# Performance work log

Measured on AMD Instinct MI355X. Metric: run time of the kernel, lower is better.

The kernel has to match this reference:

```python
import jax, jax.numpy as jnp
import numpy as np

DIM = 1024
HEADS = 16

def setup_inputs() -> dict:
    key = jax.random.key(0)
    k1, k2, k3, k4 = jax.random.split(key, 4)
    x = jax.random.normal(k1, (2, 2048, DIM), dtype=jnp.float32)
    ln_gamma = jnp.ones((DIM,), dtype=jnp.float32)
    ln_beta = jnp.zeros((DIM,), dtype=jnp.float32)
    # torch Linear weight is [out, in]; store transposed [in, out] for x @ W
    W_qkv = jax.random.normal(k2, (DIM, 3 * DIM), dtype=jnp.float32) * (DIM ** -0.5)
    W_out = jax.random.normal(k3, (DIM, DIM), dtype=jnp.float32) * (DIM ** -0.5)
    b_out = jax.random.normal(k4, (DIM,), dtype=jnp.float32) * 0.02
    return {"x": x, "ln_gamma": ln_gamma, "ln_beta": ln_beta,
            "W_qkv": W_qkv, "W_out": W_out, "b_out": b_out}

def reference(x, ln_gamma, ln_beta, W_qkv, W_out, b_out):
    B, N, C = x.shape
    H = HEADS
    Dh = C // H
    scale = Dh ** -0.5
    # LayerNorm (eps=1e-5, torch default)
    mu = jnp.mean(x, axis=-1, keepdims=True)
    var = jnp.var(x, axis=-1, keepdims=True)
    xn = (x - mu) / jnp.sqrt(var + 1e-5) * ln_gamma + ln_beta
    # QKV projection: [B,N,3C] -> [3,B,H,N,Dh]
    qkv = (xn @ W_qkv).reshape(B, N, 3, H, Dh).transpose(2, 0, 3, 1, 4)
    q, k, v = qkv[0], qkv[1], qkv[2]
    attn = jnp.einsum('bhnd,bhmd->bhnm', q, k) * scale  # [B,H,N,N]
    attn = jax.nn.softmax(attn, axis=-1)
    out = jnp.einsum('bhnm,bhmd->bhnd', attn, v)  # [B,H,N,Dh]
    out = out.transpose(0, 2, 1, 3).reshape(B, N, C)
    return out @ W_out + b_out
```

## Files before the change

kernel.cpp:

```cpp
#include <hip/hip_runtime.h>
#include <hip/hip_bf16.h>

#define DIM 1024
#define HEADS 16
#define DH 64
#define SEQ 2048
#define BATCH 2
#define ROWS (BATCH*SEQ)
#define C3 (3*DIM)
#define NT (SEQ/64)

typedef __attribute__((ext_vector_type(8))) short s16x8;
typedef __attribute__((ext_vector_type(4))) short s16x4;
typedef __attribute__((ext_vector_type(4))) float f32x4;
typedef __attribute__((ext_vector_type(16))) float f32x16;
typedef __attribute__((ext_vector_type(4))) unsigned int u32x4;
typedef __attribute__((ext_vector_type(2))) unsigned int u32x2;

__device__ __forceinline__ void gll16(const void* g, void* l) {
  __builtin_amdgcn_global_load_lds((const __attribute__((address_space(1))) void*)g,
                                   (__attribute__((address_space(3))) void*)l, 16, 0, 0);
}
__device__ __forceinline__ float bf2f(short s) {
  return __builtin_bit_cast(float, ((unsigned)(unsigned short)s) << 16);
}
__device__ __forceinline__ short f2bf(float f) {
  return (short)__bfloat16_as_ushort(__float2bfloat16(f));
}
__device__ __forceinline__ unsigned pk2(float a, float b) {
  unsigned lo = (unsigned)__bfloat16_as_ushort(__float2bfloat16(a));
  unsigned hh = (unsigned)__bfloat16_as_ushort(__float2bfloat16(b));
  return lo | (hh << 16);
}
__device__ __forceinline__ float fexp2(float x) {
#if __has_builtin(__builtin_amdgcn_exp2f)
  return __builtin_amdgcn_exp2f(x);
#else
  float r; asm("v_exp_f32 %0, %1" : "=v"(r) : "v"(x)); return r;
#endif
}

__global__ __launch_bounds__(256) void ln_kernel(const float* __restrict__ x,
    const float* __restrict__ gamma, const float* __restrict__ beta,
    __hip_bfloat16* __restrict__ xn) {
  int row = blockIdx.x;
  int t = threadIdx.x;
  const float4* xp = (const float4*)(x + (size_t)row * DIM);
  float4 v = xp[t];
  float s = v.x + v.y + v.z + v.w;
  float q = v.x*v.x + v.y*v.y + v.z*v.z + v.w*v.w;
  for (int off = 32; off >= 1; off >>= 1) {
    s += __shfl_xor(s, off, 64);
    q += __shfl_xor(q, off, 64);
  }
  __shared__ float red[8];
  int w = t >> 6;
  if ((t & 63) == 0) { red[w] = s; red[4 + w] = q; }
  __syncthreads();
  s = red[0] + red[1] + red[2] + red[3];
  q = red[4] + red[5] + red[6] + red[7];
  float mu = s * (1.0f / DIM);
  float var = q * (1.0f / DIM) - mu * mu;
  float rstd = rsqrtf(var + 1e-5f);
  int c = t * 4;
  float4 g4 = ((const float4*)gamma)[t];
  float4 b4 = ((const float4*)beta)[t];
  __hip_bfloat16* op = xn + (size_t)row * DIM + c;
  op[0] = __float2bfloat16((v.x - mu) * rstd * g4.x + b4.x);
  op[1] = __float2bfloat16((v.y - mu) * rstd * g4.y + b4.y);
  op[2] = __float2bfloat16((v.z - mu) * rstd * g4.z + b4.z);
  op[3] = __float2bfloat16((v.w - mu) * rstd * g4.w + b4.w);
}

__global__ __launch_bounds__(256) void transpose_cvt(const float* __restrict__ in,
    __hip_bfloat16* __restrict__ out, int R, int Cn) {
  __shared__ float tile[32][33];
  int c0 = blockIdx.x * 32, r0 = blockIdx.y * 32;
  int tx = threadIdx.x & 31, ty = threadIdx.x >> 5;
#pragma unroll
  for (int i = 0; i < 4; i++)
    tile[ty + i * 8][tx] = in[(size_t)(r0 + ty + i * 8) * Cn + c0 + tx];
  __syncthreads();
#pragma unroll
  for (int i = 0; i < 4; i++)
    out[(size_t)(c0 + ty + i * 8) * R + r0 + tx] = __float2bfloat16(tile[tx][ty + i * 8]);
}

__global__ __launch_bounds__(512) void gemm192(const __hip_bfloat16* __restrict__ A,
    const __hip_bfloat16* __restrict__ Bt, __hip_bfloat16* __restrict__ C,
    int M, int Nc, int K) {
  __shared__ short lds_a[2][256 * 64];
  __shared__ short lds_b[2][192 * 64];
  const int t = threadIdx.x, l = t & 63;
  const int w = t >> 6, wr = w >> 2, wc = w & 3;
  const int m0 = blockIdx.y * 256, n0 = blockIdx.x * 192;
  const short* Ab = (const short*)A;
  const short* Bb = (const short*)Bt;
  f32x4 acc[8][3] = {};
  const int srow = t >> 3;
  const int schk = (t & 7) ^ (srow & 7);
  const int NIT = K / 64;

  {
    char* la = (char*)&lds_a[0][0];
    char* lb = (char*)&lds_b[0][0];
#pragma unroll
    for (int p = 0; p < 4; p++)
      gll16(Ab + (size_t)(m0 + p * 64 + srow) * K + schk * 8, la + p * 8192 + t * 16);
#pragma unroll
    for (int p = 0; p < 3; p++)
      gll16(Bb + (size_t)(n0 + p * 64 + srow) * K + schk * 8, lb + p * 8192 + t * 16);
  }
  for (int it = 0; it < NIT; ++it) {
    const int cur = it & 1;
    __syncthreads();
    if (it + 1 < NIT) {
      const int kk = (it + 1) * 64;
      char* la = (char*)&lds_a[cur ^ 1][0];
      char* lb = (char*)&lds_b[cur ^ 1][0];
#pragma unroll
      for (int p = 0; p < 4; p++)
        gll16(Ab + (size_t)(m0 + p * 64 + srow) * K + kk + schk * 8, la + p * 8192 + t * 16);
#pragma unroll
      for (int p = 0; p < 3; p++)
        gll16(Bb + (size_t)(n0 + p * 64 + srow) * K + kk + schk * 8, lb + p * 8192 + t * 16);
      asm volatile("s_waitcnt vmcnt(7)" ::: "memory");
    } else {
      asm volatile("s_waitcnt vmcnt(0)" ::: "memory");
    }
    __syncthreads();
    const char* la = (const char*)&lds_a[cur][0];
    const char* lb = (const char*)&lds_b[cur][0];
#pragma unroll
    for (int s = 0; s < 2; s++) {
      s16x8 af[8], bf[3];
#pragma unroll
      for (int f = 0; f < 8; f++) {
        int row = wr * 128 + f * 16 + (l & 15);
        int chk = ((s * 4 + (l >> 4)) ^ (l & 7)) * 16;
        af[f] = *(const s16x8*)(la + row * 128 + chk);
      }
#pragma unroll
      for (int n = 0; n < 3; n++) {
        int row = wc * 48 + n * 16 + (l & 15);
        int chk = ((s * 4 + (l >> 4)) ^ (l & 7)) * 16;
        bf[n] = *(const s16x8*)(lb + row * 128 + chk);
      }
#pragma unroll
      for (int f = 0; f < 8; f++)
#pragma unroll
        for (int n = 0; n < 3; n++)
          acc[f][n] = __builtin_amdgcn_mfma_f32_16x16x32_bf16(af[f], bf[n], acc[f][n], 0, 0, 0);
    }
  }
#pragma unroll
  for (int f = 0; f < 8; f++)
#pragma unroll
    for (int n = 0; n < 3; n++) {
      int col = n0 + wc * 48 + n * 16 + (l & 15);
#pragma unroll
      for (int r = 0; r < 4; r++) {
        int row = m0 + wr * 128 + f * 16 + (l >> 4) * 4 + r;
        C[(size_t)row * Nc + col] = __float2bfloat16(acc[f][n][r]);
      }
    }
}

__global__ __launch_bounds__(256) void gemm_out(const __hip_bfloat16* __restrict__ A,
    const __hip_bfloat16* __restrict__ Bt, float* __restrict__ C,
    const float* __restrict__ bias) {
  __shared__ short lds_a[2][128 * 32];
  __shared__ short lds_b[2][64 * 32];
  const int t = threadIdx.x, l = t & 63, w = t >> 6;
  const int wr = w >> 1, wc = w & 1;
  const int m0 = blockIdx.y * 128, n0 = blockIdx.x * 64;
  const short* Ab = (const short*)A;
  const short* Bb = (const short*)Bt;
  const int K = DIM;
  f32x4 acc[4][2] = {};
  const int srow = t >> 2, scol = (t & 3) * 8;
  {
    char* la = (char*)&lds_a[0][0];
    char* lb = (char*)&lds_b[0][0];
    gll16(Ab + (size_t)(m0 + srow) * K + scol,      la + t * 16);
    gll16(Ab + (size_t)(m0 + 64 + srow) * K + scol, la + 4096 + t * 16);
    gll16(Bb + (size_t)(n0 + srow) * K + scol,      lb + t * 16);
  }
  for (int it = 0; it < K / 32; ++it) {
    const int cur = it & 1;
    __syncthreads();
    if (it + 1 < K / 32) {
      const int kk = (it + 1) * 32;
      char* la = (char*)&lds_a[cur ^ 1][0];
      char* lb = (char*)&lds_b[cur ^ 1][0];
      gll16(Ab + (size_t)(m0 + srow) * K + kk + scol,      la + t * 16);
      gll16(Ab + (size_t)(m0 + 64 + srow) * K + kk + scol, la + 4096 + t * 16);
      gll16(Bb + (size_t)(n0 + srow) * K + kk + scol,      lb + t * 16);
      asm volatile("s_waitcnt vmcnt(3)" ::: "memory");
    } else {
      asm volatile("s_waitcnt vmcnt(0)" ::: "memory");
    }
    __syncthreads();
    s16x8 af[4], bf[2];
#pragma unroll
    for (int m = 0; m < 4; m++)
      af[m] = *(const s16x8*)&lds_a[cur][(wr * 64 + m * 16 + (l & 15)) * 32 + (l >> 4) * 8];
#pragma unroll
    for (int n = 0; n < 2; n++)
      bf[n] = *(const s16x8*)&lds_b[cur][(wc * 32 + n * 16 + (l & 15)) * 32 + (l >> 4) * 8];
#pragma unroll
    for (int m = 0; m < 4; m++)
#pragma unroll
      for (int n = 0; n < 2; n++)
        acc[m][n] = __builtin_amdgcn_mfma_f32_16x16x32_bf16(af[m], bf[n], acc[m][n], 0, 0, 0);
  }
#pragma unroll
  for (int m = 0; m < 4; m++)
#pragma unroll
    for (int n = 0; n < 2; n++) {
      int col = n0 + wc * 32 + n * 16 + (l & 15);
      float bb = bias[col];
#pragma unroll
      for (int r = 0; r < 4; r++) {
        int row = m0 + wr * 64 + m * 16 + (l >> 4) * 4 + r;
        C[(size_t)row * DIM + col] = acc[m][n][r] + bb;
      }
    }
}

__global__ __launch_bounds__(512) void attn_kernel(const __hip_bfloat16* __restrict__ qkv,
    __hip_bfloat16* __restrict__ attno) {
  const int t = threadIdx.x, l = t & 63, w = t >> 6;
  const int hi = l >> 5, lq = l & 31;
  const int qb = blockIdx.x, bh = blockIdx.y;
  const int b = bh >> 4, h = bh & 15;
  const short* base  = (const short*)qkv + (size_t)b * SEQ * C3 + h * DH;
  const short* kbase = base + DIM;
  const short* vbase = base + 2 * DIM;
  const int qr0 = qb * 256 + w * 32;

  __shared__ short kbuf[2][64 * 64];
  __shared__ short vbuf[2][64 * 64];

  const float SCL = 0.125f * 1.44269504089f;
  s16x8 qf[4];
#pragma unroll
  for (int dk = 0; dk < 4; dk++) {
    s16x8 raw = *(const s16x8*)(base + (size_t)(qr0 + lq) * C3 + dk * 16 + hi * 8);
#pragma unroll
    for (int j = 0; j < 8; j++) qf[dk][j] = f2bf(bf2f(raw[j]) * SCL);
  }

  s16x8 ones;
#pragma unroll
  for (int j = 0; j < 8; j++) ones[j] = (short)0x3F80;

  f32x16 o0, o1, osum;
#pragma unroll
  for (int r = 0; r < 16; r++) { o0[r] = 0.f; o1[r] = 0.f; osum[r] = 0.f; }

  const int krow = t >> 3;
  const int ksrc = (t & 7) ^ (krow & 7);
  const int vr = t & 31, vcg = t >> 5;

  {
    gll16(kbase + (size_t)krow * C3 + ksrc * 8, (char*)&kbuf[0][0] + t * 16);
    u32x2 vau = __builtin_bit_cast(u32x2, *(const s16x4*)(vbase + (size_t)(2 * vr) * C3 + vcg * 4));
    u32x2 vbu = __builtin_bit_cast(u32x2, *(const s16x4*)(vbase + (size_t)(2 * vr + 1) * C3 + vcg * 4));
    char* vd = (char*)&vbuf[0][0];
#pragma unroll
    for (int i = 0; i < 4; i++) {
      int d = vcg * 4 + i;
      unsigned dw = __builtin_amdgcn_perm(vbu[i >> 1], vau[i >> 1],
                                          (i & 1) ? 0x07060302u : 0x05040100u);
      *(unsigned*)(vd + d * 128 + (((vr >> 2) ^ (d & 7)) * 16) + (vr & 3) * 4) = dw;
    }
  }
  __syncthreads();

  for (int tile = 0; tile < NT; ++tile) {
    const int cur = tile & 1;
    const bool pf = (tile + 1 < NT);
    u32x2 vau, vbu;
    if (pf) {
      const int kv1 = (tile + 1) * 64;
      gll16(kbase + (size_t)(kv1 + krow) * C3 + ksrc * 8, (char*)&kbuf[cur ^ 1][0] + t * 16);
      vau = __builtin_bit_cast(u32x2, *(const s16x4*)(vbase + (size_t)(kv1 + 2 * vr) * C3 + vcg * 4));
      vbu = __builtin_bit_cast(u32x2, *(const s16x4*)(vbase + (size_t)(kv1 + 2 * vr + 1) * C3 + vcg * 4));
    }
    const char* kb = (const char*)&kbuf[cur][0];
    f32x16 st0, st1;
#pragma unroll
    for (int r = 0; r < 16; r++) { st0[r] = 0.f; st1[r] = 0.f; }
#pragma unroll
    for (int dk = 0; dk < 4; dk++) {
      int chk = ((2 * dk + hi) ^ (l & 7)) * 16;
      s16x8 kf0 = *(const s16x8*)(kb + (size_t)lq * 128 + chk);
      s16x8 kf1 = *(const s16x8*)(kb + (size_t)(32 + lq) * 128 + chk);
      st0 = __builtin_amdgcn_mfma_f32_32x32x16_bf16(kf0, qf[dk], st0, 0, 0, 0);
      st1 = __builtin_amdgcn_mfma_f32_32x32x16_bf16(kf1, qf[dk], st1, 0, 0, 0);
    }
#pragma unroll
    for (int r = 0; r < 16; r++) {
      st0[r] = fexp2(st0[r]);
      st1[r] = fexp2(st1[r]);
    }
    const char* vbp = (const char*)&vbuf[cur][0];
#pragma unroll
    for (int n = 0; n < 2; n++) {
      const f32x16& stn = n ? st1 : st0;
#pragma unroll
      for (int ksl = 0; ksl < 2; ksl++) {
        int rb = ksl * 8;
        int a  = (int)pk2(stn[rb + 0], stn[rb + 1]);
        int bq = (int)pk2(stn[rb + 2], stn[rb + 3]);
        int c  = (int)pk2(stn[rb + 4], stn[rb + 5]);
        int d  = (int)pk2(stn[rb + 6], stn[rb + 7]);
        asm volatile("v_permlane32_swap_b32 %0, %1" : "+v"(a), "+v"(c));
        asm volatile("v_permlane32_swap_b32 %0, %1" : "+v"(bq), "+v"(d));
        u32x4 fr;
        fr.x = (unsigned)a;  fr.y = (unsigned)bq;
        fr.z = (unsigned)c;  fr.w = (unsigned)d;
        s16x8 pa = __builtin_bit_cast(s16x8, fr);
        int ks = n * 2 + ksl;
        int chk = ((2 * ks + hi) ^ (l & 7)) * 16;
        s16x8 vf0 = *(const s16x8*)(vbp + (size_t)lq * 128 + chk);
        s16x8 vf1 = *(const s16x8*)(vbp + (size_t)(32 + lq) * 128 + chk);
        o0   = __builtin_amdgcn_mfma_f32_32x32x16_bf16(pa, vf0, o0, 0, 0, 0);
        o1   = __builtin_amdgcn_mfma_f32_32x32x16_bf16(pa, vf1, o1, 0, 0, 0);
        osum = __builtin_amdgcn_mfma_f32_32x32x16_bf16(pa, ones, osum, 0, 0, 0);
      }
    }
    if (pf) {
      char* vd = (char*)&vbuf[cur ^ 1][0];
#pragma unroll
      for (int i = 0; i < 4; i++) {
        int d = vcg * 4 + i;
        unsigned dw = __builtin_amdgcn_perm(vbu[i >> 1], vau[i >> 1],
                                            (i & 1) ? 0x07060302u : 0x05040100u);
        *(unsigned*)(vd + d * 128 + (((vr >> 2) ^ (d & 7)) * 16) + (vr & 3) * 4) = dw;
      }
    }
    __syncthreads();
  }
#pragma unroll
  for (int r = 0; r < 16; r++) {
    int qr = (r & 3) + 8 * (r >> 2) + 4 * hi;
    float ir = 1.0f / osum[r];
    size_t rowoff = (size_t)(b * SEQ + qr0 + qr) * DIM + h * DH;
    attno[rowoff + lq]      = __float2bfloat16(o0[r] * ir);
    attno[rowoff + 32 + lq] = __float2bfloat16(o1[r] * ir);
  }
}

extern "C" void kernel_launch(void* const* d_in, const int* in_sizes, int n_in,
                              void* d_out, int out_size, void* d_ws, size_t ws_size,
                              hipStream_t stream) {
  const float* x     = (const float*)d_in[0];
  const float* gamma = (const float*)d_in[1];
  const float* beta  = (const float*)d_in[2];
  const float* Wqkv  = (const float*)d_in[3];
  const float* Wout  = (const float*)d_in[4];
  const float* bout  = (const float*)d_in[5];

  __hip_bfloat16* xn     = (__hip_bfloat16*)d_ws;
  __hip_bfloat16* wqkv_t = xn + (size_t)ROWS * DIM;
  __hip_bfloat16* wout_t = wqkv_t + (size_t)C3 * DIM;
  __hip_bfloat16* qkv    = wout_t + (size_t)DIM * DIM;
  __hip_bfloat16* attno  = qkv + (size_t)ROWS * C3;

  ln_kernel<<<ROWS, 256, 0, stream>>>(x, gamma, beta, xn);
  transpose_cvt<<<dim3(C3 / 32, DIM / 32), 256, 0, stream>>>(Wqkv, wqkv_t, DIM, C3);
  transpose_cvt<<<dim3(DIM / 32, DIM / 32), 256, 0, stream>>>(Wout, wout_t, DIM, DIM);
  gemm192<<<dim3(C3 / 192, ROWS / 256), 512, 0, stream>>>(xn, wqkv_t, qkv, ROWS, C3, DIM);
  attn_kernel<<<dim3(SEQ / 256, BATCH * HEADS), 512, 0, stream>>>(qkv, attno);
  gemm_out<<<dim3(DIM / 64, ROWS / 128), 256, 0, stream>>>(attno, wout_t, (float*)d_out, bout);
}
```

Measured before the change: 126.0 us.

## Merge prep kernels into one launch and split QKV GEMM inner loop into phased halves

Combines the LayerNorm and both weight transpose-convert kernels into a single prep launch, dispatching on block index, to remove two kernel launches and their gaps. Separately restructures the QKV GEMM's per-tile compute into four phases, each reading half the A fragments and then issuing MFMAs under barriers with raised wave priority. This lowers live fragment registers and interleaves LDS reads with MFMA across waves, at the cost of extra barriers per K-step.

```diff
diff --git a/kernel.cpp b/kernel.cpp
--- a/kernel.cpp
+++ b/kernel.cpp
@@ -40,50 +40,59 @@
 #endif
 }
 
-__global__ __launch_bounds__(256) void ln_kernel(const float* __restrict__ x,
+__global__ __launch_bounds__(256) void prep_kernel(const float* __restrict__ x,
     const float* __restrict__ gamma, const float* __restrict__ beta,
-    __hip_bfloat16* __restrict__ xn) {
-  int row = blockIdx.x;
-  int t = threadIdx.x;
-  const float4* xp = (const float4*)(x + (size_t)row * DIM);
-  float4 v = xp[t];
-  float s = v.x + v.y + v.z + v.w;
-  float q = v.x*v.x + v.y*v.y + v.z*v.z + v.w*v.w;
-  for (int off = 32; off >= 1; off >>= 1) {
-    s += __shfl_xor(s, off, 64);
-    q += __shfl_xor(q, off, 64);
-  }
-  __shared__ float red[8];
-  int w = t >> 6;
-  if ((t & 63) == 0) { red[w] = s; red[4 + w] = q; }
-  __syncthreads();
-  s = red[0] + red[1] + red[2] + red[3];
-  q = red[4] + red[5] + red[6] + red[7];
-  float mu = s * (1.0f / DIM);
-  float var = q * (1.0f / DIM) - mu * mu;
-  float rstd = rsqrtf(var + 1e-5f);
-  int c = t * 4;
-  float4 g4 = ((const float4*)gamma)[t];
-  float4 b4 = ((const float4*)beta)[t];
-  __hip_bfloat16* op = xn + (size_t)row * DIM + c;
-  op[0] = __float2bfloat16((v.x - mu) * rstd * g4.x + b4.x);
-  op[1] = __float2bfloat16((v.y - mu) * rstd * g4.y + b4.y);
-  op[2] = __float2bfloat16((v.z - mu) * rstd * g4.z + b4.z);
-  op[3] = __float2bfloat16((v.w - mu) * rstd * g4.w + b4.w);
-}
-
-__global__ __launch_bounds__(256) void transpose_cvt(const float* __restrict__ in,
-    __hip_bfloat16* __restrict__ out, int R, int Cn) {
-  __shared__ float tile[32][33];
-  int c0 = blockIdx.x * 32, r0 = blockIdx.y * 32;
-  int tx = threadIdx.x & 31, ty = threadIdx.x >> 5;
-#pragma unroll
-  for (int i = 0; i < 4; i++)
-    tile[ty + i * 8][tx] = in[(size_t)(r0 + ty + i * 8) * Cn + c0 + tx];
-  __syncthreads();
-#pragma unroll
-  for (int i = 0; i < 4; i++)
-    out[(size_t)(c0 + ty + i * 8) * R + r0 + tx] = __float2bfloat16(tile[tx][ty + i * 8]);
+    __hip_bfloat16* __restrict__ xn,
+    const float* __restrict__ Wqkv, __hip_bfloat16* __restrict__ wqkv_t,
+    const float* __restrict__ Wout, __hip_bfloat16* __restrict__ wout_t) {
+  const int bid = blockIdx.x;
+  const int t = threadIdx.x;
+  if (bid < ROWS) {
+    __shared__ float red[8];
+    const float4* xp = (const float4*)(x + (size_t)bid * DIM);
+    float4 v = xp[t];
+    float s = v.x + v.y + v.z + v.w;
+    float q = v.x*v.x + v.y*v.y + v.z*v.z + v.w*v.w;
+    for (int off = 32; off >= 1; off >>= 1) {
+      s += __shfl_xor(s, off, 64);
+      q += __shfl_xor(q, off, 64);
+    }
+    int w = t >> 6;
+    if ((t & 63) == 0) { red[w] = s; red[4 + w] = q; }
+    __syncthreads();
+    s = red[0] + red[1] + red[2] + red[3];
+    q = red[4] + red[5] + red[6] + red[7];
+    float mu = s * (1.0f / DIM);
+    float var = q * (1.0f / DIM) - mu * mu;
+    float rstd = rsqrtf(var + 1e-5f);
+    float4 g4 = ((const float4*)gamma)[t];
+    float4 b4 = ((const float4*)beta)[t];
+    __hip_bfloat16* op = xn + (size_t)bid * DIM + t * 4;
+    op[0] = __float2bfloat16((v.x - mu) * rstd * g4.x + b4.x);
+    op[1] = __float2bfloat16((v.y - mu) * rstd * g4.y + b4.y);
+    op[2] = __float2bfloat16((v.z - mu) * rstd * g4.z + b4.z);
+    op[3] = __float2bfloat16((v.w - mu) * rstd * g4.w + b4.w);
+  } else {
+    __shared__ float tile[32][33];
+    const float* in; __hip_bfloat16* out; int R, Cn, c0, r0;
+    if (bid < ROWS + 3072) {
+      int id = bid - ROWS;
+      in = Wqkv; out = wqkv_t; R = DIM; Cn = C3;
+      c0 = (id % 96) * 32; r0 = (id / 96) * 32;
+    } else {
+      int id = bid - ROWS - 3072;
+      in = Wout; out = wout_t; R = DIM; Cn = DIM;
+      c0 = (id % 32) * 32; r0 = (id / 32) * 32;
+    }
+    int tx = t & 31, ty = t >> 5;
+#pragma unroll
+    for (int i = 0; i < 4; i++)
+      tile[ty + i * 8][tx] = in[(size_t)(r0 + ty + i * 8) * Cn + c0 + tx];
+    __syncthreads();
+#pragma unroll
+    for (int i = 0; i < 4; i++)
+      out[(size_t)(c0 + ty + i * 8) * R + r0 + tx] = __float2bfloat16(tile[tx][ty + i * 8]);
+  }
 }
 
 __global__ __launch_bounds__(512) void gemm192(const __hip_bfloat16* __restrict__ A,
@@ -131,27 +140,43 @@
     __syncthreads();
     const char* la = (const char*)&lds_a[cur][0];
     const char* lb = (const char*)&lds_b[cur][0];
-#pragma unroll
-    for (int s = 0; s < 2; s++) {
-      s16x8 af[8], bf[3];
-#pragma unroll
-      for (int f = 0; f < 8; f++) {
-        int row = wr * 128 + f * 16 + (l & 15);
-        int chk = ((s * 4 + (l >> 4)) ^ (l & 7)) * 16;
-        af[f] = *(const s16x8*)(la + row * 128 + chk);
-      }
-#pragma unroll
-      for (int n = 0; n < 3; n++) {
-        int row = wc * 48 + n * 16 + (l & 15);
-        int chk = ((s * 4 + (l >> 4)) ^ (l & 7)) * 16;
-        bf[n] = *(const s16x8*)(lb + row * 128 + chk);
-      }
-#pragma unroll
-      for (int f = 0; f < 8; f++)
-#pragma unroll
-        for (int n = 0; n < 3; n++)
-          acc[f][n] = __builtin_amdgcn_mfma_f32_16x16x32_bf16(af[f], bf[n], acc[f][n], 0, 0, 0);
-    }
+    s16x8 af[4], bf[3];
+#define GPH_READ_A(FH, S)                                                     \
+    _Pragma("unroll")                                                         \
+    for (int f = 0; f < 4; f++) {                                             \
+      int row = wr * 128 + (FH * 4 + f) * 16 + (l & 15);                      \
+      int chk = (((S) * 4 + (l >> 4)) ^ (l & 7)) * 16;                        \
+      af[f] = *(const s16x8*)(la + row * 128 + chk);                          \
+    }
+#define GPH_READ_B(S)                                                         \
+    _Pragma("unroll")                                                         \
+    for (int n = 0; n < 3; n++) {                                             \
+      int row = wc * 48 + n * 16 + (l & 15);                                  \
+      int chk = (((S) * 4 + (l >> 4)) ^ (l & 7)) * 16;                        \
+      bf[n] = *(const s16x8*)(lb + row * 128 + chk);                          \
+    }
+#define GPH_MFMA(FH)                                                          \
+    __builtin_amdgcn_s_barrier();                                             \
+    asm volatile("s_waitcnt lgkmcnt(0)" ::: "memory");                        \
+    __builtin_amdgcn_sched_barrier(0);                                        \
+    __builtin_amdgcn_s_setprio(1);                                            \
+    _Pragma("unroll")                                                         \
+    for (int f = 0; f < 4; f++)                                               \
+      _Pragma("unroll")                                                       \
+      for (int n = 0; n < 3; n++)                                             \
+        acc[FH * 4 + f][n] =                                                  \
+            __builtin_amdgcn_mfma_f32_16x16x32_bf16(af[f], bf[n],             \
+                                                    acc[FH * 4 + f][n], 0, 0, 0); \
+    __builtin_amdgcn_s_setprio(0);                                            \
+    __builtin_amdgcn_s_barrier();
+
+    GPH_READ_A(0, 0) GPH_READ_B(0) GPH_MFMA(0)
+    GPH_READ_A(1, 0) GPH_MFMA(1)
+    GPH_READ_A(0, 1) GPH_READ_B(1) GPH_MFMA(0)
+    GPH_READ_A(1, 1) GPH_MFMA(1)
+#undef GPH_READ_A
+#undef GPH_READ_B
+#undef GPH_MFMA
   }
 #pragma unroll
   for (int f = 0; f < 8; f++)
@@ -369,9 +394,8 @@
   __hip_bfloat16* qkv    = wout_t + (size_t)DIM * DIM;
   __hip_bfloat16* attno  = qkv + (size_t)ROWS * C3;
 
-  ln_kernel<<<ROWS, 256, 0, stream>>>(x, gamma, beta, xn);
-  transpose_cvt<<<dim3(C3 / 32, DIM / 32), 256, 0, stream>>>(Wqkv, wqkv_t, DIM, C3);
-  transpose_cvt<<<dim3(DIM / 32, DIM / 32), 256, 0, stream>>>(Wout, wout_t, DIM, DIM);
+  prep_kernel<<<ROWS + 3072 + 1024, 256, 0, stream>>>(x, gamma, beta, xn,
+                                                      Wqkv, wqkv_t, Wout, wout_t);
   gemm192<<<dim3(C3 / 192, ROWS / 256), 512, 0, stream>>>(xn, wqkv_t, qkv, ROWS, C3, DIM);
   attn_kernel<<<dim3(SEQ / 256, BATCH * HEADS), 512, 0, stream>>>(qkv, attno);
   gemm_out<<<dim3(DIM / 64, ROWS / 128), 256, 0, stream>>>(attno, wout_t, (float*)d_out, bout);
```

Result: no change. 124.8 us (-1.0%).
